# Kernel tuning notes

Measured on AMD Instinct MI355X. Metric: run time of the kernel, lower is better.

The kernel has to match this reference:

```python
import jax, jax.numpy as jnp
import numpy as np

N_NODES = 100000
N_EDGES = 1600000
IN_DIM = 128
HID = 64
N_GRAPHS = 1024
EPS = 1e-5


def setup_inputs() -> dict:
    key = jax.random.key(0)
    ks = jax.random.split(key, 16)
    x = jax.random.normal(ks[0], (N_NODES, IN_DIM), dtype=jnp.float32)
    edge_index = jax.random.randint(ks[1], (2, N_EDGES), 0, N_NODES, dtype=jnp.int32)
    batch = jnp.sort(jax.random.randint(ks[2], (N_NODES,), 0, N_GRAPHS, dtype=jnp.int32))
    def glorot(k, shape):
        lim = np.sqrt(6.0 / (shape[0] + shape[1]))
        return jax.random.uniform(k, shape, jnp.float32, -lim, lim)
    return {
        'x': x, 'edge_index': edge_index, 'batch': batch,
        'w1': glorot(ks[3], (IN_DIM, HID)), 'b1': jnp.zeros((HID,), jnp.float32),
        'g1': jnp.ones((HID,), jnp.float32), 'be1': jnp.zeros((HID,), jnp.float32),
        'w2': glorot(ks[4], (HID, HID)), 'b2': jnp.zeros((HID,), jnp.float32),
        'g2': jnp.ones((HID,), jnp.float32), 'be2': jnp.zeros((HID,), jnp.float32),
        'w3': glorot(ks[5], (HID, HID)), 'b3': jnp.zeros((HID,), jnp.float32),
        'g3': jnp.ones((HID,), jnp.float32), 'be3': jnp.zeros((HID,), jnp.float32),
        'fc_w': glorot(ks[6], (HID, 1)), 'fc_b': jnp.zeros((1,), jnp.float32),
    }


def _batch_norm(h, gamma, beta):
    # training-mode BN over the node dimension (biased variance, as torch)
    mean = jnp.mean(h, axis=0)
    var = jnp.mean((h - mean) ** 2, axis=0)
    return (h - mean) * jax.lax.rsqrt(var + EPS) * gamma + beta


def reference(x, edge_index, batch, w1, b1, g1, be1, w2, b2, g2, be2,
              w3, b3, g3, be3, fc_w, fc_b):
    n = x.shape[0]
    # GCN normalization with added self-loops (PyG GCNConv semantics)
    loop = jnp.arange(n, dtype=edge_index.dtype)
    row = jnp.concatenate([edge_index[0], loop])  # source
    col = jnp.concatenate([edge_index[1], loop])  # target
    deg = jax.ops.segment_sum(jnp.ones_like(col, dtype=x.dtype), col, num_segments=n)
    dinv = jnp.where(deg > 0, jax.lax.rsqrt(deg), 0.0)
    norm = (dinv[row] * dinv[col])[:, None]  # [E+N, 1]

    def gcn(h, W, b):
        m = h @ W                                   # [N, HID]
        agg = jax.ops.segment_sum(m[row] * norm, col, num_segments=n)
        return agg + b

    h = jax.nn.relu(_batch_norm(gcn(x, w1, b1), g1, be1))
    res = h  # dropout is identity in eval mode
    h = jax.nn.relu(_batch_norm(gcn(h, w2, b2), g2, be2) + res)
    h = jax.nn.relu(_batch_norm(gcn(h, w3, b3), g3, be3))

    # global mean pool over graphs
    sums = jax.ops.segment_sum(h, batch, num_segments=N_GRAPHS)
    cnt = jax.ops.segment_sum(jnp.ones((n,), x.dtype), batch, num_segments=N_GRAPHS)
    pooled = sums / jnp.maximum(cnt, 1.0)[:, None]
    return (pooled @ fc_w + fc_b).squeeze(-1)  # [N_GRAPHS]
```

## Files before the change

### kernel.cpp

```cpp
#include <hip/hip_runtime.h>

#define NN 100000
#define NE 1600000
#define INDIM 128
#define HID 64
#define NG 1024
#define NB 1563
#define SCB 256
#define EPB ((NE + SCB - 1) / SCB)
#define SEGCAP 2048
#define BN_EPS 1e-5f

typedef unsigned short u16;
typedef unsigned int u32;

__device__ __forceinline__ u16 f2bf(float f) {
    u32 u = __float_as_uint(f);
    u32 r = (u + 0x7fffu + ((u >> 16) & 1u)) >> 16;
    return (u16)r;
}
__device__ __forceinline__ float bf2f(u32 b) {
    return __uint_as_float(b << 16);
}


__global__ void k_hist(const int* __restrict__ col, int* __restrict__ hist, int E) {
    __shared__ int h[NB];
    int b = blockIdx.x;
    for (int i = threadIdx.x; i < NB; i += 256) h[i] = 0;
    __syncthreads();
    int s = b * EPB, e = min(s + EPB, E);
    for (int i = s + threadIdx.x; i < e; i += 256) {
        atomicAdd(&h[col[i] >> 6], 1);
    }
    __syncthreads();
    for (int i = threadIdx.x; i < NB; i += 256) hist[b * NB + i] = h[i];
}

__global__ void k_btot(const int* __restrict__ hist, int* __restrict__ bcnt) {
    int t = blockIdx.x * 256 + threadIdx.x;
    if (t < NB) {
        int s = 0;
        for (int b = 0; b < SCB; b++) s += hist[b * NB + t];
        bcnt[t] = s;
    }
}

__global__ void k_bscan(const int* __restrict__ bcnt, int* __restrict__ bstart, int B, int E) {
    __shared__ int ts[256];
    int t = threadIdx.x;
    int loc[7];
    int s = 0;
    for (int i = 0; i < 7; i++) {
        int idx = t * 7 + i;
        loc[i] = (idx < B) ? bcnt[idx] : 0;
        s += loc[i];
    }
    ts[t] = s;
    __syncthreads();
    for (int off = 1; off < 256; off <<= 1) {
        int add = (t >= off) ? ts[t - off] : 0;
        __syncthreads();
        ts[t] += add;
        __syncthreads();
    }
    int ex = ts[t] - s;
    for (int i = 0; i < 7; i++) {
        int idx = t * 7 + i;
        if (idx < B) bstart[idx] = ex;
        ex += loc[i];
    }
    if (t == 0) bstart[B] = E;
}

__global__ void k_hcol(int* __restrict__ hist, const int* __restrict__ bstart) {
    int t = blockIdx.x * 256 + threadIdx.x;
    if (t < NB) {
        int run = bstart[t];
        for (int b = 0; b < SCB; b++) {
            int idx = b * NB + t;
            int v = hist[idx];
            hist[idx] = run;
            run += v;
        }
    }
}

__global__ void k_scatter(const int* __restrict__ row, const int* __restrict__ col,
                          const int* __restrict__ hist, u32* __restrict__ ebuf, int E) {
    __shared__ int cur[NB];
    int b = blockIdx.x;
    for (int i = threadIdx.x; i < NB; i += 256) cur[i] = hist[b * NB + i];
    __syncthreads();
    int s = b * EPB, e = min(s + EPB, E);
    for (int i = s + threadIdx.x; i < e; i += 256) {
        int c = col[i];
        int p = atomicAdd(&cur[c >> 6], 1);
        ebuf[p] = ((u32)row[i] << 6) | (u32)(c & 63);
    }
}

__global__ void __launch_bounds__(256)
k_csr(const u32* __restrict__ ebuf, const int* __restrict__ bstart,
      u32* __restrict__ glrows, int* __restrict__ goffs,
      float* __restrict__ dinv, int N) {
    __shared__ u32 seg[SEGCAP];
    __shared__ int lcnt[64], lstart[64], lcur[64];
    int b = blockIdx.x, t = threadIdx.x;
    int lane = t & 63, w = t >> 6;
    int s = bstart[b];
    int cnt = min(bstart[b + 1] - s, SEGCAP);
    if (t < 64) { lcnt[t] = 0; lcur[t] = 0; }
    __syncthreads();
    for (int i = t; i < cnt; i += 256) {
        u32 v = ebuf[s + i];
        seg[i] = v;
        atomicAdd(&lcnt[v & 63u], 1);
    }
    __syncthreads();
    if (w == 0) {
        int v = lcnt[lane];
        int x = v;
        for (int o = 1; o < 64; o <<= 1) {
            int y = __shfl_up(x, o, 64);
            if (lane >= o) x += y;
        }
        lstart[lane] = x - v;
    }
    __syncthreads();
    for (int i = t; i < cnt; i += 256) {
        u32 v = seg[i];
        int c = (int)(v & 63u);
        int p = s + lstart[c] + atomicAdd(&lcur[c], 1);
        glrows[p] = v >> 6;
    }
    if (t < 64) {
        int node = b * 64 + t;
        if (node < N) {
            goffs[node] = s + lstart[t];
            dinv[node] = rsqrtf((float)(lcnt[t] + 1));
        } else if (node == N) {
            goffs[N] = s + lstart[t];
        }
    }
}


template<int K>
__global__ void k_gemm(const float* __restrict__ h, const float* __restrict__ W,
                       const float* __restrict__ dinv, u16* __restrict__ m, int N,
                       const float* __restrict__ bnStats, const float* __restrict__ bnG,
                       const float* __restrict__ bnB) {
    __shared__ float sh[16][K];
    const float invN = 1.0f / (float)N;
    const int K4 = K / 4;
    int block0 = blockIdx.x * 16;
    for (int idx = threadIdx.x; idx < 16 * K4; idx += 256) {
        int nn = idx / K4, kk4 = idx % K4;
        int node = block0 + nn;
        float4 v = make_float4(0.f, 0.f, 0.f, 0.f);
        if (node < N) v = *(const float4*)(h + (size_t)node * K + kk4 * 4);
        if (bnStats) {
            #pragma unroll
            for (int j = 0; j < 4; j++) {
                int kk = kk4 * 4 + j;
                float mean = bnStats[kk] * invN;
                float var = bnStats[K + kk] * invN - mean * mean;
                float sc = bnG[kk] * rsqrtf(var + BN_EPS);
                float* pv = (j == 0) ? &v.x : (j == 1) ? &v.y : (j == 2) ? &v.z : &v.w;
                *pv = fmaxf((*pv - mean) * sc + bnB[kk], 0.f);
            }
        }
        *(float4*)(&sh[nn][kk4 * 4]) = v;
    }
    __syncthreads();
    int colj = threadIdx.x & 63;
    int nl = threadIdx.x >> 6;
    float a0 = 0.f, a1 = 0.f, a2 = 0.f, a3 = 0.f;
    #pragma unroll 8
    for (int k = 0; k < K; k++) {
        float w = W[k * HID + colj];
        a0 += sh[nl][k] * w;
        a1 += sh[nl + 4][k] * w;
        a2 += sh[nl + 8][k] * w;
        a3 += sh[nl + 12][k] * w;
    }
    int n0 = block0 + nl;
    if (n0 < N)      m[(size_t)n0 * HID + colj]        = f2bf(a0 * dinv[n0]);
    if (n0 + 4 < N)  m[(size_t)(n0 + 4) * HID + colj]  = f2bf(a1 * dinv[n0 + 4]);
    if (n0 + 8 < N)  m[(size_t)(n0 + 8) * HID + colj]  = f2bf(a2 * dinv[n0 + 8]);
    if (n0 + 12 < N) m[(size_t)(n0 + 12) * HID + colj] = f2bf(a3 * dinv[n0 + 12]);
}

__global__ void k_gemm3(const float* __restrict__ agg1, const float* __restrict__ agg2,
                        const float* __restrict__ st1, const float* __restrict__ st2,
                        const float* __restrict__ g1, const float* __restrict__ be1,
                        const float* __restrict__ g2, const float* __restrict__ be2,
                        const float* __restrict__ W, const float* __restrict__ dinv,
                        u16* __restrict__ m, int N) {
    __shared__ float sh[16][HID];
    const float invN = 1.0f / (float)N;
    int block0 = blockIdx.x * 16;
    for (int idx = threadIdx.x; idx < 16 * 16; idx += 256) {
        int nn = idx / 16, kk4 = idx % 16;
        int node = block0 + nn;
        float4 o = make_float4(0.f, 0.f, 0.f, 0.f);
        if (node < N) {
            size_t p = (size_t)node * HID + kk4 * 4;
            float4 v1 = *(const float4*)(agg1 + p);
            float4 v2 = *(const float4*)(agg2 + p);
            float* p1 = &v1.x; float* p2 = &v2.x; float* po = &o.x;
            #pragma unroll
            for (int j = 0; j < 4; j++) {
                int kk = kk4 * 4 + j;
                float m1 = st1[kk] * invN;
                float va1 = st1[64 + kk] * invN - m1 * m1;
                float s1 = g1[kk] * rsqrtf(va1 + BN_EPS);
                float h1 = fmaxf((p1[j] - m1) * s1 + be1[kk], 0.f);
                float m2 = st2[kk] * invN;
                float va2 = st2[64 + kk] * invN - m2 * m2;
                float s2 = g2[kk] * rsqrtf(va2 + BN_EPS);
                po[j] = fmaxf((p2[j] - m2) * s2 + be2[kk] + h1, 0.f);
            }
        }
        *(float4*)(&sh[nn][kk4 * 4]) = o;
    }
    __syncthreads();
    int colj = threadIdx.x & 63;
    int nl = threadIdx.x >> 6;
    float a0 = 0.f, a1 = 0.f, a2 = 0.f, a3 = 0.f;
    #pragma unroll 8
    for (int k = 0; k < HID; k++) {
        float w = W[k * HID + colj];
        a0 += sh[nl][k] * w;
        a1 += sh[nl + 4][k] * w;
        a2 += sh[nl + 8][k] * w;
        a3 += sh[nl + 12][k] * w;
    }
    int n0 = block0 + nl;
    if (n0 < N)      m[(size_t)n0 * HID + colj]        = f2bf(a0 * dinv[n0]);
    if (n0 + 4 < N)  m[(size_t)(n0 + 4) * HID + colj]  = f2bf(a1 * dinv[n0 + 4]);
    if (n0 + 8 < N)  m[(size_t)(n0 + 8) * HID + colj]  = f2bf(a2 * dinv[n0 + 8]);
    if (n0 + 12 < N) m[(size_t)(n0 + 12) * HID + colj] = f2bf(a3 * dinv[n0 + 12]);
}

__global__ void __launch_bounds__(256)
k_fusedagg(const u16* __restrict__ m, const float* __restrict__ dinv,
           const u32* __restrict__ glrows, const int* __restrict__ goffs,
           float* __restrict__ agg, float* __restrict__ stats, int N) {
    __shared__ float rs[4][32], rq[4][32];
    int b = blockIdx.x, hh = blockIdx.y;
    int t = threadIdx.x;
    int lane = t & 63, w = t >> 6;
    int g = lane >> 3;
    int sub = lane & 7;
    int qidx = hh * 8 + sub;
    int node0 = b * 64;
    float ssum[4] = {0.f, 0.f, 0.f, 0.f}, ssq[4] = {0.f, 0.f, 0.f, 0.f};
    for (int i = 0; i < 16; i++) {
        int node = node0 + w * 16 + i;
        if (node >= N) continue;
        float a0 = 0.f, a1 = 0.f, a2 = 0.f, a3 = 0.f;
        if (g == 0) {
            uint2 v = ((const uint2*)(m + ((size_t)node << 6)))[qidx];
            a0 = bf2f(v.x & 0xffffu); a1 = bf2f(v.x >> 16);
            a2 = bf2f(v.y & 0xffffu); a3 = bf2f(v.y >> 16);
        }
        int s = goffs[node], e = goffs[node + 1];
        #pragma unroll 2
        for (int k = s + g; k < e; k += 8) {
            int r = (int)glrows[k];
            uint2 v = ((const uint2*)(m + ((size_t)r << 6)))[qidx];
            a0 += bf2f(v.x & 0xffffu); a1 += bf2f(v.x >> 16);
            a2 += bf2f(v.y & 0xffffu); a3 += bf2f(v.y >> 16);
        }
        a0 += __shfl_xor(a0, 8, 64); a0 += __shfl_xor(a0, 16, 64); a0 += __shfl_xor(a0, 32, 64);
        a1 += __shfl_xor(a1, 8, 64); a1 += __shfl_xor(a1, 16, 64); a1 += __shfl_xor(a1, 32, 64);
        a2 += __shfl_xor(a2, 8, 64); a2 += __shfl_xor(a2, 16, 64); a2 += __shfl_xor(a2, 32, 64);
        a3 += __shfl_xor(a3, 8, 64); a3 += __shfl_xor(a3, 16, 64); a3 += __shfl_xor(a3, 32, 64);
        if (lane < 8) {
            float di = dinv[node];
            float v0 = a0 * di, v1 = a1 * di, v2 = a2 * di, v3 = a3 * di;
            *(float4*)(agg + ((size_t)node << 6) + hh * 32 + sub * 4) =
                make_float4(v0, v1, v2, v3);
            ssum[0] += v0; ssum[1] += v1; ssum[2] += v2; ssum[3] += v3;
            ssq[0] += v0 * v0; ssq[1] += v1 * v1; ssq[2] += v2 * v2; ssq[3] += v3 * v3;
        }
    }
    if (lane < 8) {
        #pragma unroll
        for (int j = 0; j < 4; j++) {
            rs[w][sub * 4 + j] = ssum[j];
            rq[w][sub * 4 + j] = ssq[j];
        }
    }
    __syncthreads();
    if (w == 0 && lane < 32) {
        float a = rs[0][lane] + rs[1][lane] + rs[2][lane] + rs[3][lane];
        float q = rq[0][lane] + rq[1][lane] + rq[2][lane] + rq[3][lane];
        atomicAdd(&stats[hh * 32 + lane], a);
        atomicAdd(&stats[64 + hh * 32 + lane], q);
    }
}

__global__ void k_pool(const float* __restrict__ agg3, const float* __restrict__ st3,
                       const float* __restrict__ g3, const float* __restrict__ be3,
                       const int* __restrict__ batch, float* __restrict__ pooled,
                       float* __restrict__ gcnt, int N) {
    int lane = threadIdx.x;
    int start = blockIdx.x * 64;
    if (start >= N) return;
    const float invN = 1.0f / (float)N;
    float mean = st3[lane] * invN;
    float var = st3[64 + lane] * invN - mean * mean;
    float sc = g3[lane] * rsqrtf(var + BN_EPS);
    float bb = be3[lane];
    int end = min(start + 64, N);
    int gcur = batch[start];
    float acc = 0.f; int run = 0;
    for (int n = start; n < end; n++) {
        int g = batch[n];
        if (g != gcur) {
            atomicAdd(&pooled[gcur * HID + lane], acc);
            if (lane == 0) atomicAdd(&gcnt[gcur], (float)run);
            acc = 0.f; run = 0; gcur = g;
        }
        acc += fmaxf((agg3[(size_t)n * HID + lane] - mean) * sc + bb, 0.f);
        run++;
    }
    atomicAdd(&pooled[gcur * HID + lane], acc);
    if (lane == 0) atomicAdd(&gcnt[gcur], (float)run);
}

__global__ void k_final(const float* __restrict__ pooled, const float* __restrict__ gcnt,
                        const float* __restrict__ fcw, const float* __restrict__ fcb,
                        float* __restrict__ out) {
    int g = (int)((blockIdx.x * (size_t)blockDim.x + threadIdx.x) >> 6);
    int lane = threadIdx.x & 63;
    if (g >= NG) return;
    float c = fmaxf(gcnt[g], 1.f);
    float v = pooled[g * HID + lane] / c * fcw[lane];
    for (int off = 32; off > 0; off >>= 1) v += __shfl_down(v, off, 64);
    if (lane == 0) out[g] = v + fcb[0];
}


extern "C" void kernel_launch(void* const* d_in, const int* in_sizes, int n_in,
                              void* d_out, int out_size, void* d_ws, size_t ws_size,
                              hipStream_t stream) {
    const float* x    = (const float*)d_in[0];
    const int*   ei   = (const int*)d_in[1];
    const int*   batch= (const int*)d_in[2];
    const float* w1   = (const float*)d_in[3];
    const float* g1   = (const float*)d_in[5];
    const float* be1  = (const float*)d_in[6];
    const float* w2   = (const float*)d_in[7];
    const float* g2   = (const float*)d_in[9];
    const float* be2  = (const float*)d_in[10];
    const float* w3   = (const float*)d_in[11];
    const float* g3   = (const float*)d_in[13];
    const float* be3  = (const float*)d_in[14];
    const float* fcw  = (const float*)d_in[15];
    const float* fcb  = (const float*)d_in[16];
    float* out = (float*)d_out;

    const int N = NN, E = NE;
    const int* erow = ei;
    const int* ecol = ei + E;

    char* ws = (char*)d_ws;
    size_t off = 0;
    auto alloc = [&](size_t bytes) -> char* {
        char* p = ws + off;
        off = (off + bytes + 255) & ~(size_t)255;
        return p;
    };
    float* dinv   = (float*)alloc((size_t)N * 4);
    int*   hist   = (int*)alloc((size_t)SCB * NB * 4);
    int*   bcnt   = (int*)alloc((size_t)NB * 4);
    int*   bstart = (int*)alloc((size_t)(NB + 1) * 4);
    u32*   ebuf   = (u32*)alloc((size_t)E * 4);
    u32*   glrows = (u32*)alloc((size_t)E * 4);
    int*   goffs  = (int*)alloc((size_t)(N + 1) * 4);
    u16*   bufM   = (u16*)alloc((size_t)N * HID * 2);
    float* aggB1  = (float*)alloc((size_t)N * HID * 4);
    float* aggB2  = (float*)alloc((size_t)N * HID * 4);
    float* stats  = (float*)alloc(3 * 128 * 4);
    float* pooled = (float*)alloc((size_t)NG * HID * 4);
    float* gcnt   = (float*)alloc((size_t)NG * 4);
    (void)ws_size; (void)in_sizes; (void)n_in; (void)out_size;

    float* aggB3 = aggB1;

    hipMemsetAsync(stats, 0, 3 * 128 * 4, stream);
    hipMemsetAsync(pooled, 0, (size_t)NG * HID * 4, stream);
    hipMemsetAsync(gcnt, 0, (size_t)NG * 4, stream);

    const int nbNode16 = (N + 15) / 16;
    const int nbB = (NB + 255) / 256;
    dim3 aggGrid(NB, 2);

    k_hist<<<SCB, 256, 0, stream>>>(ecol, hist, E);
    k_btot<<<nbB, 256, 0, stream>>>(hist, bcnt);
    k_bscan<<<1, 256, 0, stream>>>(bcnt, bstart, NB, E);
    k_hcol<<<nbB, 256, 0, stream>>>(hist, bstart);
    k_scatter<<<SCB, 256, 0, stream>>>(erow, ecol, hist, ebuf, E);
    k_csr<<<NB, 256, 0, stream>>>(ebuf, bstart, glrows, goffs, dinv, N);

    k_gemm<INDIM><<<nbNode16, 256, 0, stream>>>(x, w1, dinv, bufM, N,
                                                nullptr, nullptr, nullptr);
    k_fusedagg<<<aggGrid, 256, 0, stream>>>(bufM, dinv, glrows, goffs, aggB1, stats, N);

    k_gemm<HID><<<nbNode16, 256, 0, stream>>>(aggB1, w2, dinv, bufM, N,
                                              stats, g1, be1);
    k_fusedagg<<<aggGrid, 256, 0, stream>>>(bufM, dinv, glrows, goffs, aggB2, stats + 128, N);

    k_gemm3<<<nbNode16, 256, 0, stream>>>(aggB1, aggB2, stats, stats + 128,
                                          g1, be1, g2, be2, w3, dinv, bufM, N);
    k_fusedagg<<<aggGrid, 256, 0, stream>>>(bufM, dinv, glrows, goffs, aggB3, stats + 256, N);

    k_pool<<<(N + 63) / 64, 64, 0, stream>>>(aggB3, stats + 256, g3, be3,
                                             batch, pooled, gcnt, N);
    k_final<<<(NG * 64) / 256, 256, 0, stream>>>(pooled, gcnt, fcw, fcb, out);
}
```

Measured before the change: 605.4 us.

## Store aggregation outputs in bf16 and gather full feature rows per block

```diff
diff --git a/kernel.cpp b/kernel.cpp
--- a/kernel.cpp
+++ b/kernel.cpp
@@ -148,11 +148,8 @@
 
 template<int K>
 __global__ void k_gemm(const float* __restrict__ h, const float* __restrict__ W,
-                       const float* __restrict__ dinv, u16* __restrict__ m, int N,
-                       const float* __restrict__ bnStats, const float* __restrict__ bnG,
-                       const float* __restrict__ bnB) {
+                       const float* __restrict__ dinv, u16* __restrict__ m, int N) {
     __shared__ float sh[16][K];
-    const float invN = 1.0f / (float)N;
     const int K4 = K / 4;
     int block0 = blockIdx.x * 16;
     for (int idx = threadIdx.x; idx < 16 * K4; idx += 256) {
@@ -160,17 +157,6 @@
         int node = block0 + nn;
         float4 v = make_float4(0.f, 0.f, 0.f, 0.f);
         if (node < N) v = *(const float4*)(h + (size_t)node * K + kk4 * 4);
-        if (bnStats) {
-            #pragma unroll
-            for (int j = 0; j < 4; j++) {
-                int kk = kk4 * 4 + j;
-                float mean = bnStats[kk] * invN;
-                float var = bnStats[K + kk] * invN - mean * mean;
-                float sc = bnG[kk] * rsqrtf(var + BN_EPS);
-                float* pv = (j == 0) ? &v.x : (j == 1) ? &v.y : (j == 2) ? &v.z : &v.w;
-                *pv = fmaxf((*pv - mean) * sc + bnB[kk], 0.f);
-            }
-        }
         *(float4*)(&sh[nn][kk4 * 4]) = v;
     }
     __syncthreads();
@@ -192,38 +178,34 @@
     if (n0 + 12 < N) m[(size_t)(n0 + 12) * HID + colj] = f2bf(a3 * dinv[n0 + 12]);
 }
 
-__global__ void k_gemm3(const float* __restrict__ agg1, const float* __restrict__ agg2,
-                        const float* __restrict__ st1, const float* __restrict__ st2,
-                        const float* __restrict__ g1, const float* __restrict__ be1,
-                        const float* __restrict__ g2, const float* __restrict__ be2,
-                        const float* __restrict__ W, const float* __restrict__ dinv,
-                        u16* __restrict__ m, int N) {
+__global__ void k_gemm2(const u16* __restrict__ h, const float* __restrict__ W,
+                        const float* __restrict__ dinv, u16* __restrict__ m, int N,
+                        const float* __restrict__ st, const float* __restrict__ bnG,
+                        const float* __restrict__ bnB) {
     __shared__ float sh[16][HID];
     const float invN = 1.0f / (float)N;
     int block0 = blockIdx.x * 16;
-    for (int idx = threadIdx.x; idx < 16 * 16; idx += 256) {
-        int nn = idx / 16, kk4 = idx % 16;
+    for (int idx = threadIdx.x; idx < 16 * 8; idx += 256) {
+        int nn = idx >> 3, k8 = idx & 7;
         int node = block0 + nn;
-        float4 o = make_float4(0.f, 0.f, 0.f, 0.f);
+        float vals[8] = {0.f, 0.f, 0.f, 0.f, 0.f, 0.f, 0.f, 0.f};
         if (node < N) {
-            size_t p = (size_t)node * HID + kk4 * 4;
-            float4 v1 = *(const float4*)(agg1 + p);
-            float4 v2 = *(const float4*)(agg2 + p);
-            float* p1 = &v1.x; float* p2 = &v2.x; float* po = &o.x;
+            uint4 v = ((const uint4*)(h + ((size_t)node << 6)))[k8];
+            vals[0] = bf2f(v.x & 0xffffu); vals[1] = bf2f(v.x >> 16);
+            vals[2] = bf2f(v.y & 0xffffu); vals[3] = bf2f(v.y >> 16);
+            vals[4] = bf2f(v.z & 0xffffu); vals[5] = bf2f(v.z >> 16);
+            vals[6] = bf2f(v.w & 0xffffu); vals[7] = bf2f(v.w >> 16);
             #pragma unroll
-            for (int j = 0; j < 4; j++) {
-                int kk = kk4 * 4 + j;
-                float m1 = st1[kk] * invN;
-                float va1 = st1[64 + kk] * invN - m1 * m1;
-                float s1 = g1[kk] * rsqrtf(va1 + BN_EPS);
-                float h1 = fmaxf((p1[j] - m1) * s1 + be1[kk], 0.f);
-                float m2 = st2[kk] * invN;
-                float va2 = st2[64 + kk] * invN - m2 * m2;
-                float s2 = g2[kk] * rsqrtf(va2 + BN_EPS);
-                po[j] = fmaxf((p2[j] - m2) * s2 + be2[kk] + h1, 0.f);
+            for (int j = 0; j < 8; j++) {
+                int kk = k8 * 8 + j;
+                float mean = st[kk] * invN;
+                float var = st[64 + kk] * invN - mean * mean;
+                float sc = bnG[kk] * rsqrtf(var + BN_EPS);
+                vals[j] = fmaxf((vals[j] - mean) * sc + bnB[kk], 0.f);
             }
         }
-        *(float4*)(&sh[nn][kk4 * 4]) = o;
+        *(float4*)(&sh[nn][k8 * 8])     = make_float4(vals[0], vals[1], vals[2], vals[3]);
+        *(float4*)(&sh[nn][k8 * 8 + 4]) = make_float4(vals[4], vals[5], vals[6], vals[7]);
     }
     __syncthreads();
     int colj = threadIdx.x & 63;
@@ -244,50 +226,109 @@
     if (n0 + 12 < N) m[(size_t)(n0 + 12) * HID + colj] = f2bf(a3 * dinv[n0 + 12]);
 }
 
+__global__ void k_gemm3(const u16* __restrict__ agg1, const u16* __restrict__ agg2,
+                        const float* __restrict__ st1, const float* __restrict__ st2,
+                        const float* __restrict__ g1, const float* __restrict__ be1,
+                        const float* __restrict__ g2, const float* __restrict__ be2,
+                        const float* __restrict__ W, const float* __restrict__ dinv,
+                        u16* __restrict__ m, int N) {
+    __shared__ float sh[16][HID];
+    const float invN = 1.0f / (float)N;
+    int block0 = blockIdx.x * 16;
+    for (int idx = threadIdx.x; idx < 16 * 8; idx += 256) {
+        int nn = idx >> 3, k8 = idx & 7;
+        int node = block0 + nn;
+        float o[8] = {0.f, 0.f, 0.f, 0.f, 0.f, 0.f, 0.f, 0.f};
+        if (node < N) {
+            uint4 v1 = ((const uint4*)(agg1 + ((size_t)node << 6)))[k8];
+            uint4 v2 = ((const uint4*)(agg2 + ((size_t)node << 6)))[k8];
+            float a1v[8], a2v[8];
+            a1v[0] = bf2f(v1.x & 0xffffu); a1v[1] = bf2f(v1.x >> 16);
+            a1v[2] = bf2f(v1.y & 0xffffu); a1v[3] = bf2f(v1.y >> 16);
+            a1v[4] = bf2f(v1.z & 0xffffu); a1v[5] = bf2f(v1.z >> 16);
+            a1v[6] = bf2f(v1.w & 0xffffu); a1v[7] = bf2f(v1.w >> 16);
+            a2v[0] = bf2f(v2.x & 0xffffu); a2v[1] = bf2f(v2.x >> 16);
+            a2v[2] = bf2f(v2.y & 0xffffu); a2v[3] = bf2f(v2.y >> 16);
+            a2v[4] = bf2f(v2.z & 0xffffu); a2v[5] = bf2f(v2.z >> 16);
+            a2v[6] = bf2f(v2.w & 0xffffu); a2v[7] = bf2f(v2.w >> 16);
+            #pragma unroll
+            for (int j = 0; j < 8; j++) {
+                int kk = k8 * 8 + j;
+                float m1 = st1[kk] * invN;
+                float va1 = st1[64 + kk] * invN - m1 * m1;
+                float s1 = g1[kk] * rsqrtf(va1 + BN_EPS);
+                float h1 = fmaxf((a1v[j] - m1) * s1 + be1[kk], 0.f);
+                float m2 = st2[kk] * invN;
+                float va2 = st2[64 + kk] * invN - m2 * m2;
+                float s2 = g2[kk] * rsqrtf(va2 + BN_EPS);
+                o[j] = fmaxf((a2v[j] - m2) * s2 + be2[kk] + h1, 0.f);
+            }
+        }
+        *(float4*)(&sh[nn][k8 * 8])     = make_float4(o[0], o[1], o[2], o[3]);
+        *(float4*)(&sh[nn][k8 * 8 + 4]) = make_float4(o[4], o[5], o[6], o[7]);
+    }
+    __syncthreads();
+    int colj = threadIdx.x & 63;
+    int nl = threadIdx.x >> 6;
+    float a0 = 0.f, a1 = 0.f, a2 = 0.f, a3 = 0.f;
+    #pragma unroll 8
+    for (int k = 0; k < HID; k++) {
+        float w = W[k * HID + colj];
+        a0 += sh[nl][k] * w;
+        a1 += sh[nl + 4][k] * w;
+        a2 += sh[nl + 8][k] * w;
+        a3 += sh[nl + 12][k] * w;
+    }
+    int n0 = block0 + nl;
+    if (n0 < N)      m[(size_t)n0 * HID + colj]        = f2bf(a0 * dinv[n0]);
+    if (n0 + 4 < N)  m[(size_t)(n0 + 4) * HID + colj]  = f2bf(a1 * dinv[n0 + 4]);
+    if (n0 + 8 < N)  m[(size_t)(n0 + 8) * HID + colj]  = f2bf(a2 * dinv[n0 + 8]);
+    if (n0 + 12 < N) m[(size_t)(n0 + 12) * HID + colj] = f2bf(a3 * dinv[n0 + 12]);
+}
+
 __global__ void __launch_bounds__(256)
-k_fusedagg(const u16* __restrict__ m, const float* __restrict__ dinv,
-           const u32* __restrict__ glrows, const int* __restrict__ goffs,
-           float* __restrict__ agg, float* __restrict__ stats, int N) {
-    __shared__ float rs[4][32], rq[4][32];
-    int b = blockIdx.x, hh = blockIdx.y;
+k_agg(const u16* __restrict__ m, const float* __restrict__ dinv,
+      const u32* __restrict__ glrows, const int* __restrict__ goffs,
+      u16* __restrict__ agg, float* __restrict__ stats, int N) {
+    __shared__ float rs[4][64], rq[4][64];
     int t = threadIdx.x;
     int lane = t & 63, w = t >> 6;
-    int g = lane >> 3;
-    int sub = lane & 7;
-    int qidx = hh * 8 + sub;
-    int node0 = b * 64;
+    int g = lane >> 4;
+    int sub = lane & 15;
+    int node0 = blockIdx.x * 64;
     float ssum[4] = {0.f, 0.f, 0.f, 0.f}, ssq[4] = {0.f, 0.f, 0.f, 0.f};
     for (int i = 0; i < 16; i++) {
         int node = node0 + w * 16 + i;
         if (node >= N) continue;
         float a0 = 0.f, a1 = 0.f, a2 = 0.f, a3 = 0.f;
         if (g == 0) {
-            uint2 v = ((const uint2*)(m + ((size_t)node << 6)))[qidx];
+            uint2 v = ((const uint2*)(m + ((size_t)node << 6)))[sub];
             a0 = bf2f(v.x & 0xffffu); a1 = bf2f(v.x >> 16);
             a2 = bf2f(v.y & 0xffffu); a3 = bf2f(v.y >> 16);
         }
         int s = goffs[node], e = goffs[node + 1];
         #pragma unroll 2
-        for (int k = s + g; k < e; k += 8) {
+        for (int k = s + g; k < e; k += 4) {
             int r = (int)glrows[k];
-            uint2 v = ((const uint2*)(m + ((size_t)r << 6)))[qidx];
+            uint2 v = ((const uint2*)(m + ((size_t)r << 6)))[sub];
             a0 += bf2f(v.x & 0xffffu); a1 += bf2f(v.x >> 16);
             a2 += bf2f(v.y & 0xffffu); a3 += bf2f(v.y >> 16);
         }
-        a0 += __shfl_xor(a0, 8, 64); a0 += __shfl_xor(a0, 16, 64); a0 += __shfl_xor(a0, 32, 64);
-        a1 += __shfl_xor(a1, 8, 64); a1 += __shfl_xor(a1, 16, 64); a1 += __shfl_xor(a1, 32, 64);
-        a2 += __shfl_xor(a2, 8, 64); a2 += __shfl_xor(a2, 16, 64); a2 += __shfl_xor(a2, 32, 64);
-        a3 += __shfl_xor(a3, 8, 64); a3 += __shfl_xor(a3, 16, 64); a3 += __shfl_xor(a3, 32, 64);
-        if (lane < 8) {
+        a0 += __shfl_xor(a0, 16, 64); a0 += __shfl_xor(a0, 32, 64);
+        a1 += __shfl_xor(a1, 16, 64); a1 += __shfl_xor(a1, 32, 64);
+        a2 += __shfl_xor(a2, 16, 64); a2 += __shfl_xor(a2, 32, 64);
+        a3 += __shfl_xor(a3, 16, 64); a3 += __shfl_xor(a3, 32, 64);
+        if (lane < 16) {
             float di = dinv[node];
             float v0 = a0 * di, v1 = a1 * di, v2 = a2 * di, v3 = a3 * di;
-            *(float4*)(agg + ((size_t)node << 6) + hh * 32 + sub * 4) =
-                make_float4(v0, v1, v2, v3);
+            u32 lo = (u32)f2bf(v0) | ((u32)f2bf(v1) << 16);
+            u32 hi = (u32)f2bf(v2) | ((u32)f2bf(v3) << 16);
+            ((uint2*)(agg + ((size_t)node << 6)))[sub] = make_uint2(lo, hi);
             ssum[0] += v0; ssum[1] += v1; ssum[2] += v2; ssum[3] += v3;
             ssq[0] += v0 * v0; ssq[1] += v1 * v1; ssq[2] += v2 * v2; ssq[3] += v3 * v3;
         }
     }
-    if (lane < 8) {
+    if (lane < 16) {
         #pragma unroll
         for (int j = 0; j < 4; j++) {
             rs[w][sub * 4 + j] = ssum[j];
@@ -295,15 +336,15 @@
         }
     }
     __syncthreads();
-    if (w == 0 && lane < 32) {
+    if (w == 0) {
         float a = rs[0][lane] + rs[1][lane] + rs[2][lane] + rs[3][lane];
         float q = rq[0][lane] + rq[1][lane] + rq[2][lane] + rq[3][lane];
-        atomicAdd(&stats[hh * 32 + lane], a);
-        atomicAdd(&stats[64 + hh * 32 + lane], q);
-    }
-}
-
-__global__ void k_pool(const float* __restrict__ agg3, const float* __restrict__ st3,
+        atomicAdd(&stats[lane], a);
+        atomicAdd(&stats[64 + lane], q);
+    }
+}
+
+__global__ void k_pool(const u16* __restrict__ agg3, const float* __restrict__ st3,
                        const float* __restrict__ g3, const float* __restrict__ be3,
                        const int* __restrict__ batch, float* __restrict__ pooled,
                        float* __restrict__ gcnt, int N) {
@@ -325,7 +366,8 @@
             if (lane == 0) atomicAdd(&gcnt[gcur], (float)run);
             acc = 0.f; run = 0; gcur = g;
         }
-        acc += fmaxf((agg3[(size_t)n * HID + lane] - mean) * sc + bb, 0.f);
+        float v = bf2f((u32)agg3[(size_t)n * HID + lane]);
+        acc += fmaxf((v - mean) * sc + bb, 0.f);
         run++;
     }
     atomicAdd(&pooled[gcur * HID + lane], acc);
@@ -383,14 +425,14 @@
     u32*   glrows = (u32*)alloc((size_t)E * 4);
     int*   goffs  = (int*)alloc((size_t)(N + 1) * 4);
     u16*   bufM   = (u16*)alloc((size_t)N * HID * 2);
-    float* aggB1  = (float*)alloc((size_t)N * HID * 4);
-    float* aggB2  = (float*)alloc((size_t)N * HID * 4);
+    u16*   aggB1  = (u16*)alloc((size_t)N * HID * 2);
+    u16*   aggB2  = (u16*)alloc((size_t)N * HID * 2);
     float* stats  = (float*)alloc(3 * 128 * 4);
     float* pooled = (float*)alloc((size_t)NG * HID * 4);
     float* gcnt   = (float*)alloc((size_t)NG * 4);
     (void)ws_size; (void)in_sizes; (void)n_in; (void)out_size;
 
-    float* aggB3 = aggB1;
+    u16* aggB3 = aggB1;
 
     hipMemsetAsync(stats, 0, 3 * 128 * 4, stream);
     hipMemsetAsync(pooled, 0, (size_t)NG * HID * 4, stream);
@@ -398,7 +440,6 @@
 
     const int nbNode16 = (N + 15) / 16;
     const int nbB = (NB + 255) / 256;
-    dim3 aggGrid(NB, 2);
 
     k_hist<<<SCB, 256, 0, stream>>>(ecol, hist, E);
     k_btot<<<nbB, 256, 0, stream>>>(hist, bcnt);
@@ -407,17 +448,16 @@
     k_scatter<<<SCB, 256, 0, stream>>>(erow, ecol, hist, ebuf, E);
     k_csr<<<NB, 256, 0, stream>>>(ebuf, bstart, glrows, goffs, dinv, N);
 
-    k_gemm<INDIM><<<nbNode16, 256, 0, stream>>>(x, w1, dinv, bufM, N,
-                                                nullptr, nullptr, nullptr);
-    k_fusedagg<<<aggGrid, 256, 0, stream>>>(bufM, dinv, glrows, goffs, aggB1, stats, N);
-
-    k_gemm<HID><<<nbNode16, 256, 0, stream>>>(aggB1, w2, dinv, bufM, N,
-                                              stats, g1, be1);
-    k_fusedagg<<<aggGrid, 256, 0, stream>>>(bufM, dinv, glrows, goffs, aggB2, stats + 128, N);
+    k_gemm<INDIM><<<nbNode16, 256, 0, stream>>>(x, w1, dinv, bufM, N);
+    k_agg<<<NB, 256, 0, stream>>>(bufM, dinv, glrows, goffs, aggB1, stats, N);
+
+    k_gemm2<<<nbNode16, 256, 0, stream>>>(aggB1, w2, dinv, bufM, N,
+                                          stats, g1, be1);
+    k_agg<<<NB, 256, 0, stream>>>(bufM, dinv, glrows, goffs, aggB2, stats + 128, N);
 
     k_gemm3<<<nbNode16, 256, 0, stream>>>(aggB1, aggB2, stats, stats + 128,
                                           g1, be1, g2, be2, w3, dinv, bufM, N);
-    k_fusedagg<<<aggGrid, 256, 0, stream>>>(bufM, dinv, glrows, goffs, aggB3, stats + 256, N);
+    k_agg<<<NB, 256, 0, stream>>>(bufM, dinv, glrows, goffs, aggB3, stats + 256, N);
 
     k_pool<<<(N + 63) / 64, 64, 0, stream>>>(aggB3, stats + 256, g3, be3,
                                              batch, pooled, gcnt, N);
```

New measurement: 550.5 us. 1.1x faster.
